# Optimization experiments

Hardware: AMD Instinct MI355X
Metric: run time of the kernel (lower is better)

## Reference

```python
import jax, jax.numpy as jnp
import numpy as np

B, N, F_IN = 8, 1024, 256
N_HEADS, N_HIDDEN = 8, 32  # out_features=256, is_concat=True -> n_hidden = 256//8
NEG_SLOPE = 0.2


def setup_inputs() -> dict:
    key = jax.random.key(0)
    k1, k2, k3 = jax.random.split(key, 3)
    vertex = jax.random.normal(k1, (B, N, F_IN), dtype=jnp.float32)
    # linear_vert.weight.T  (applied as x @ w_vert)
    w_vert = jax.random.normal(k2, (F_IN, N_HEADS * N_HIDDEN), dtype=jnp.float32) / np.sqrt(F_IN)
    # attn linear: [2*n_hidden] -> 1, no bias; shared across heads
    attn_w = jax.random.normal(k3, (2 * N_HIDDEN,), dtype=jnp.float32) / np.sqrt(2 * N_HIDDEN)
    return {"vertex": vertex, "w_vert": w_vert, "attn_w": attn_w}


def reference(vertex, w_vert, attn_w):
    b, n, _ = vertex.shape
    # g_vertex: [b, n, h, d]
    g = jnp.einsum("bni,io->bno", vertex, w_vert).reshape(b, n, N_HEADS, N_HIDDEN)
    # attn(cat([g_i, g_j])) == g_i . w_src + g_j . w_dst  (cat index i = repeat_interleave half)
    w_src, w_dst = attn_w[:N_HIDDEN], attn_w[N_HIDDEN:]
    s_src = jnp.einsum("bnhd,d->bnh", g, w_src)  # [b, n, h]
    s_dst = jnp.einsum("bnhd,d->bnh", g, w_dst)  # [b, n, h]
    # e[b,i,j,h] = LeakyReLU(s_src[b,i,h] + s_dst[b,j,h])
    e = s_src[:, :, None, :] + s_dst[:, None, :, :]
    e = jnp.where(e >= 0, e, NEG_SLOPE * e)
    # softmax over j (dim=-2 after squeeze in the torch code)
    a = jax.nn.softmax(e, axis=2)  # [b, i, j, h]
    # dropout in eval mode = identity
    out = jnp.einsum("bijh,bjhd->bihd", a, g)  # [b, n, h, d]
    return out.reshape(b, n, N_HEADS * N_HIDDEN)
```

## Files before the change

kernel.cpp:

```cpp
#include <hip/hip_runtime.h>
#include <hip/hip_bf16.h>
#include <math.h>

#define F_IN  256
#define NOUT  256
#define NB    8
#define NN    1024
#define NH    8
#define ND    32
#define NROWS (NB * NN)
#define LOG2E 1.44269504f

typedef __attribute__((ext_vector_type(8))) short bf16x8;
typedef __attribute__((ext_vector_type(4))) float f32x4;

__device__ inline unsigned pk_bf16(float a, float b) {
    union { __hip_bfloat162 h2; unsigned u; } c;
    c.h2 = __float22bfloat162_rn(make_float2(a, b));
    return c.u;
}
__device__ inline unsigned short bf16u(float a) {
    union { __hip_bfloat16 h; unsigned short u; } c;
    c.h = __float2bfloat16(a);
    return c.u;
}
__device__ inline float bf2f(unsigned short u) {
    union { unsigned u; float f; } c;
    c.u = ((unsigned)u) << 16;
    return c.f;
}
__device__ inline void split8(const float4 va, const float4 vb,
                              bf16x8& hi, bf16x8& lo) {
    float f[8] = {va.x, va.y, va.z, va.w, vb.x, vb.y, vb.z, vb.w};
    union { bf16x8 v; unsigned u[4]; } H, L;
    #pragma unroll
    for (int i = 0; i < 4; ++i) {
        unsigned short h0 = bf16u(f[2 * i]);
        unsigned short h1 = bf16u(f[2 * i + 1]);
        H.u[i] = (unsigned)h0 | ((unsigned)h1 << 16);
        L.u[i] = pk_bf16(f[2 * i] - bf2f(h0), f[2 * i + 1] - bf2f(h1));
    }
    hi = H.v; lo = L.v;
}

__global__ __launch_bounds__(256) void w_prep_kernel(
    const float* __restrict__ w_vert,
    unsigned short* __restrict__ wT_hi, unsigned short* __restrict__ wT_lo)
{
    __shared__ float wf[64][68];
    const int t  = threadIdx.x;
    const int kt = (blockIdx.x >> 2) * 64;
    const int nt = (blockIdx.x & 3) * 64;
    #pragma unroll
    for (int q = 0; q < 4; ++q) {
        const int kr = (t >> 4) + 16 * q;
        const int nc = (t & 15) * 4;
        float4 v = *(const float4*)&w_vert[(size_t)(kt + kr) * NOUT + nt + nc];
        wf[kr][nc + 0] = v.x; wf[kr][nc + 1] = v.y;
        wf[kr][nc + 2] = v.z; wf[kr][nc + 3] = v.w;
    }
    __syncthreads();
    const int n = t >> 2, ks = (t & 3) * 16;
    unsigned Hs[8], Ls[8];
    #pragma unroll
    for (int i = 0; i < 8; ++i) {
        float x0 = wf[ks + 2 * i][n], x1 = wf[ks + 2 * i + 1][n];
        unsigned short h0 = bf16u(x0), h1 = bf16u(x1);
        Hs[i] = (unsigned)h0 | ((unsigned)h1 << 16);
        Ls[i] = pk_bf16(x0 - bf2f(h0), x1 - bf2f(h1));
    }
    unsigned* ph = (unsigned*)(wT_hi + (size_t)(nt + n) * F_IN + kt + ks);
    unsigned* pl = (unsigned*)(wT_lo + (size_t)(nt + n) * F_IN + kt + ks);
    #pragma unroll
    for (int i = 0; i < 8; ++i) { ph[i] = Hs[i]; pl[i] = Ls[i]; }
}

__global__ __launch_bounds__(256) void gat_gemm_kernel(
    const float* __restrict__ vertex,
    const unsigned short* __restrict__ wT_hi,
    const unsigned short* __restrict__ wT_lo,
    const float* __restrict__ attn_w, unsigned short* __restrict__ gT,
    float* __restrict__ ssT, float* __restrict__ sdT)
{
    __shared__ f32x4 comb[2][4][64];
    const int t = threadIdx.x, lane = t & 63, wv = t >> 6;
    const int mt = wv & 1, kh = wv >> 1;
    const int il = lane & 15, ql = lane >> 4;
    const int h = blockIdx.x, gr0 = blockIdx.y * 64;
    const int b = gr0 >> 10, bh = b * NH + h;

    const float* arow0 = vertex + (size_t)(gr0 + mt * 32 + il) * F_IN + kh * 128 + ql * 8;
    const float* arow1 = arow0 + 16 * F_IN;
    const unsigned short* b0h = wT_hi + (size_t)(h * 32 + il) * F_IN + kh * 128 + ql * 8;
    const unsigned short* b1h = b0h + 16 * F_IN;
    const unsigned short* b0l = wT_lo + (size_t)(h * 32 + il) * F_IN + kh * 128 + ql * 8;
    const unsigned short* b1l = b0l + 16 * F_IN;

    f32x4 c00 = {0.f, 0.f, 0.f, 0.f}, c01 = c00, c10 = c00, c11 = c00;

    #pragma unroll 2
    for (int kk = 0; kk < 128; kk += 32) {
        float4 a0a = *(const float4*)(arow0 + kk);
        float4 a0b = *(const float4*)(arow0 + kk + 4);
        float4 a1a = *(const float4*)(arow1 + kk);
        float4 a1b = *(const float4*)(arow1 + kk + 4);
        bf16x8 bh0 = *(const bf16x8*)(b0h + kk);
        bf16x8 bh1 = *(const bf16x8*)(b1h + kk);
        bf16x8 bl0 = *(const bf16x8*)(b0l + kk);
        bf16x8 bl1 = *(const bf16x8*)(b1l + kk);

        bf16x8 a0hi, a0lo, a1hi, a1lo;
        split8(a0a, a0b, a0hi, a0lo);
        split8(a1a, a1b, a1hi, a1lo);

        c00 = __builtin_amdgcn_mfma_f32_16x16x32_bf16(a0hi, bh0, c00, 0, 0, 0);
        c01 = __builtin_amdgcn_mfma_f32_16x16x32_bf16(a0hi, bh1, c01, 0, 0, 0);
        c10 = __builtin_amdgcn_mfma_f32_16x16x32_bf16(a1hi, bh0, c10, 0, 0, 0);
        c11 = __builtin_amdgcn_mfma_f32_16x16x32_bf16(a1hi, bh1, c11, 0, 0, 0);
        c00 = __builtin_amdgcn_mfma_f32_16x16x32_bf16(a0lo, bh0, c00, 0, 0, 0);
        c01 = __builtin_amdgcn_mfma_f32_16x16x32_bf16(a0lo, bh1, c01, 0, 0, 0);
        c10 = __builtin_amdgcn_mfma_f32_16x16x32_bf16(a1lo, bh0, c10, 0, 0, 0);
        c11 = __builtin_amdgcn_mfma_f32_16x16x32_bf16(a1lo, bh1, c11, 0, 0, 0);
        c00 = __builtin_amdgcn_mfma_f32_16x16x32_bf16(a0hi, bl0, c00, 0, 0, 0);
        c01 = __builtin_amdgcn_mfma_f32_16x16x32_bf16(a0hi, bl1, c01, 0, 0, 0);
        c10 = __builtin_amdgcn_mfma_f32_16x16x32_bf16(a1hi, bl0, c10, 0, 0, 0);
        c11 = __builtin_amdgcn_mfma_f32_16x16x32_bf16(a1hi, bl1, c11, 0, 0, 0);
    }

    if (kh == 1) {
        comb[mt][0][lane] = c00; comb[mt][1][lane] = c01;
        comb[mt][2][lane] = c10; comb[mt][3][lane] = c11;
    }
    __syncthreads();
    if (kh == 0) {
        c00 = c00 + comb[mt][0][lane]; c01 = c01 + comb[mt][1][lane];
        c10 = c10 + comb[mt][2][lane]; c11 = c11 + comb[mt][3][lane];

        const int j0 = (gr0 & 1023) + mt * 32;
        const float wsv0 = attn_w[il],      wsv1 = attn_w[16 + il];
        const float wdv0 = attn_w[ND + il], wdv1 = attn_w[ND + 16 + il];

        #pragma unroll
        for (int g = 0; g < 2; ++g) {
            f32x4 cA = g ? c10 : c00;
            f32x4 cB = g ? c11 : c01;
            const int jr = j0 + g * 16 + ql * 4;

            unsigned g2[2];
            g2[0] = pk_bf16(cA[0], cA[1]); g2[1] = pk_bf16(cA[2], cA[3]);
            *(uint2*)(gT + ((size_t)(bh * ND) + il) * NN + jr) = *(uint2*)g2;
            g2[0] = pk_bf16(cB[0], cB[1]); g2[1] = pk_bf16(cB[2], cB[3]);
            *(uint2*)(gT + ((size_t)(bh * ND) + 16 + il) * NN + jr) = *(uint2*)g2;

            #pragma unroll
            for (int reg = 0; reg < 4; ++reg) {
                float ps = cA[reg] * wsv0 + cB[reg] * wsv1;
                float pd = cA[reg] * wdv0 + cB[reg] * wdv1;
                #pragma unroll
                for (int off = 1; off < 16; off <<= 1) {
                    ps += __shfl_xor(ps, off);
                    pd += __shfl_xor(pd, off);
                }
                if (il == 0) {
                    ssT[bh * NN + jr + reg] = ps;
                    sdT[bh * NN + jr + reg] = pd;
                }
            }
        }
    }
}

__global__ __launch_bounds__(256, 4) void gat_attn_kernel(
    const unsigned short* __restrict__ gT, const float* __restrict__ ssT,
    const float* __restrict__ sdT, float* __restrict__ out)
{
    __shared__ __align__(16) float Bp[NN];
    __shared__ __align__(16) float Bn[NN];
    __shared__ f32x4 ccomb[2][12][64];
    __shared__ float red[4];

    const int bid = blockIdx.x;
    const int bh = bid & 63;
    const int b = bh >> 3, h = bh & 7;
    const int i0 = (bid >> 6) * 64;
    const int t = threadIdx.x, lane = t & 63, jq = t >> 6;
    const int il = lane & 15, ql = lane >> 4;

    float sdv[4]; float M = -3.0e38f;
    #pragma unroll
    for (int q = 0; q < 4; ++q) {
        sdv[q] = sdT[bh * NN + t + 256 * q];
        M = fmaxf(M, sdv[q]);
    }
    #pragma unroll
    for (int off = 32; off >= 1; off >>= 1)
        M = fmaxf(M, __shfl_xor(M, off));
    if (lane == 0) red[jq] = M;
    #pragma unroll
    for (int q = 0; q < 4; ++q) {
        Bp[t + 256 * q] = exp2f(sdv[q] * LOG2E);
        Bn[t + 256 * q] = exp2f(0.2f * LOG2E * sdv[q]);
    }
    __syncthreads();
    M = fmaxf(fmaxf(red[0], red[1]), fmaxf(red[2], red[3]));

    float Ap[4], An[4];
    #pragma unroll
    for (int mt = 0; mt < 4; ++mt) {
        const float si = ssT[bh * NN + i0 + mt * 16 + il];
        float x = si + M; x = fmaxf(x, 0.2f * x);
        const float mk = x * LOG2E;
        Ap[mt] = exp2f(fmaf(si, LOG2E, -mk));
        An[mt] = exp2f(fmaf(0.2f * si, LOG2E, -mk));
    }

    const unsigned short* gb0 = gT + ((size_t)(bh * ND) + il) * NN + jq * 256 + ql * 8;
    const unsigned short* gb1 = gb0 + 16 * NN;
    const float* bpq = Bp + jq * 256 + ql * 8;
    const float* bnq = Bn + jq * 256 + ql * 8;

    union { bf16x8 v; unsigned u[4]; } ones;
    ones.u[0] = ones.u[1] = ones.u[2] = ones.u[3] = 0x3F803F80u;

    f32x4 c0[4], c1[4], cs[4];
    #pragma unroll
    for (int mt = 0; mt < 4; ++mt) {
        c0[mt] = (f32x4){0.f, 0.f, 0.f, 0.f};
        c1[mt] = c0[mt]; cs[mt] = c0[mt];
    }

    #pragma unroll 2
    for (int kk = 0; kk < 256; kk += 32) {
        const float4 p0 = *(const float4*)(bpq + kk);
        const float4 p1 = *(const float4*)(bpq + kk + 4);
        const float4 n0 = *(const float4*)(bnq + kk);
        const float4 n1 = *(const float4*)(bnq + kk + 4);
        const bf16x8 bf0 = *(const bf16x8*)(gb0 + kk);
        const bf16x8 bf1 = *(const bf16x8*)(gb1 + kk);

        float pv[8] = {p0.x, p0.y, p0.z, p0.w, p1.x, p1.y, p1.z, p1.w};
        float nv[8] = {n0.x, n0.y, n0.z, n0.w, n1.x, n1.y, n1.z, n1.w};

        #pragma unroll
        for (int mt = 0; mt < 4; ++mt) {
            float e[8];
            #pragma unroll
            for (int u = 0; u < 8; ++u)
                e[u] = fmaxf(Ap[mt] * pv[u], An[mt] * nv[u]);
            union { bf16x8 v; unsigned u[4]; } af;
            #pragma unroll
            for (int u = 0; u < 4; ++u)
                af.u[u] = pk_bf16(e[2 * u], e[2 * u + 1]);
            c0[mt] = __builtin_amdgcn_mfma_f32_16x16x32_bf16(af.v, bf0, c0[mt], 0, 0, 0);
            c1[mt] = __builtin_amdgcn_mfma_f32_16x16x32_bf16(af.v, bf1, c1[mt], 0, 0, 0);
            cs[mt] = __builtin_amdgcn_mfma_f32_16x16x32_bf16(af.v, ones.v, cs[mt], 0, 0, 0);
        }
    }

    if (jq >= 2) {
        #pragma unroll
        for (int mt = 0; mt < 4; ++mt) {
            ccomb[jq - 2][mt * 3 + 0][lane] = c0[mt];
            ccomb[jq - 2][mt * 3 + 1][lane] = c1[mt];
            ccomb[jq - 2][mt * 3 + 2][lane] = cs[mt];
        }
    }
    __syncthreads();
    if (jq < 2) {
        #pragma unroll
        for (int mt = 0; mt < 4; ++mt) {
            c0[mt] = c0[mt] + ccomb[jq][mt * 3 + 0][lane];
            c1[mt] = c1[mt] + ccomb[jq][mt * 3 + 1][lane];
            cs[mt] = cs[mt] + ccomb[jq][mt * 3 + 2][lane];
        }
    }
    __syncthreads();
    if (jq == 1) {
        #pragma unroll
        for (int mt = 0; mt < 4; ++mt) {
            ccomb[0][mt * 3 + 0][lane] = c0[mt];
            ccomb[0][mt * 3 + 1][lane] = c1[mt];
            ccomb[0][mt * 3 + 2][lane] = cs[mt];
        }
    }
    __syncthreads();
    if (jq == 0) {
        #pragma unroll
        for (int mt = 0; mt < 4; ++mt) {
            c0[mt] = c0[mt] + ccomb[0][mt * 3 + 0][lane];
            c1[mt] = c1[mt] + ccomb[0][mt * 3 + 1][lane];
            cs[mt] = cs[mt] + ccomb[0][mt * 3 + 2][lane];

            float* ob = out + (size_t)(b * NN + i0 + mt * 16 + ql * 4) * NOUT + h * ND + il;
            #pragma unroll
            for (int reg = 0; reg < 4; ++reg) {
                const float r = 1.0f / cs[mt][reg];
                ob[reg * NOUT]      = c0[mt][reg] * r;
                ob[reg * NOUT + 16] = c1[mt][reg] * r;
            }
        }
    }
}

extern "C" void kernel_launch(void* const* d_in, const int* in_sizes, int n_in,
                              void* d_out, int out_size, void* d_ws, size_t ws_size,
                              hipStream_t stream) {
    (void)in_sizes; (void)n_in; (void)out_size; (void)ws_size;
    const float* vertex = (const float*)d_in[0];
    const float* w_vert = (const float*)d_in[1];
    const float* attn_w = (const float*)d_in[2];
    float* out = (float*)d_out;

    char* ws = (char*)d_ws;
    unsigned short* wT_hi = (unsigned short*)ws;
    unsigned short* wT_lo = (unsigned short*)(ws + (128 << 10));
    unsigned short* gT    = (unsigned short*)(ws + (256 << 10));
    float* ssT = (float*)(ws + (256 << 10) + ((size_t)NB * NH * ND * NN * 2));
    float* sdT = ssT + (size_t)NB * NH * NN;

    w_prep_kernel<<<16, 256, 0, stream>>>(w_vert, wT_hi, wT_lo);
    gat_gemm_kernel<<<dim3(NH, 128), 256, 0, stream>>>(vertex, wT_hi, wT_lo,
                                                       attn_w, gT, ssT, sdT);
    gat_attn_kernel<<<1024, 256, 0, stream>>>(gT, ssT, sdT, out);
}
```

Before: 96.72 us.

## Fuse weight bf16 split into GEMM kernel via shared-memory staging

```diff
diff --git a/kernel.cpp b/kernel.cpp
--- a/kernel.cpp
+++ b/kernel.cpp
@@ -43,71 +43,66 @@
     hi = H.v; lo = L.v;
 }
 
-__global__ __launch_bounds__(256) void w_prep_kernel(
-    const float* __restrict__ w_vert,
-    unsigned short* __restrict__ wT_hi, unsigned short* __restrict__ wT_lo)
-{
-    __shared__ float wf[64][68];
-    const int t  = threadIdx.x;
-    const int kt = (blockIdx.x >> 2) * 64;
-    const int nt = (blockIdx.x & 3) * 64;
-    #pragma unroll
-    for (int q = 0; q < 4; ++q) {
-        const int kr = (t >> 4) + 16 * q;
-        const int nc = (t & 15) * 4;
-        float4 v = *(const float4*)&w_vert[(size_t)(kt + kr) * NOUT + nt + nc];
-        wf[kr][nc + 0] = v.x; wf[kr][nc + 1] = v.y;
-        wf[kr][nc + 2] = v.z; wf[kr][nc + 3] = v.w;
-    }
-    __syncthreads();
-    const int n = t >> 2, ks = (t & 3) * 16;
-    unsigned Hs[8], Ls[8];
-    #pragma unroll
-    for (int i = 0; i < 8; ++i) {
-        float x0 = wf[ks + 2 * i][n], x1 = wf[ks + 2 * i + 1][n];
-        unsigned short h0 = bf16u(x0), h1 = bf16u(x1);
-        Hs[i] = (unsigned)h0 | ((unsigned)h1 << 16);
-        Ls[i] = pk_bf16(x0 - bf2f(h0), x1 - bf2f(h1));
-    }
-    unsigned* ph = (unsigned*)(wT_hi + (size_t)(nt + n) * F_IN + kt + ks);
-    unsigned* pl = (unsigned*)(wT_lo + (size_t)(nt + n) * F_IN + kt + ks);
-    #pragma unroll
-    for (int i = 0; i < 8; ++i) { ph[i] = Hs[i]; pl[i] = Ls[i]; }
-}
-
 __global__ __launch_bounds__(256) void gat_gemm_kernel(
-    const float* __restrict__ vertex,
-    const unsigned short* __restrict__ wT_hi,
-    const unsigned short* __restrict__ wT_lo,
+    const float* __restrict__ vertex, const float* __restrict__ w_vert,
     const float* __restrict__ attn_w, unsigned short* __restrict__ gT,
     float* __restrict__ ssT, float* __restrict__ sdT)
 {
-    __shared__ f32x4 comb[2][4][64];
+    __shared__ __align__(16) unsigned short bHi[8192];
+    __shared__ __align__(16) unsigned short bLo[8192];
+    f32x4 (*comb)[4][64] = reinterpret_cast<f32x4(*)[4][64]>(bHi);
+
     const int t = threadIdx.x, lane = t & 63, wv = t >> 6;
     const int mt = wv & 1, kh = wv >> 1;
     const int il = lane & 15, ql = lane >> 4;
     const int h = blockIdx.x, gr0 = blockIdx.y * 64;
     const int b = gr0 >> 10, bh = b * NH + h;
 
+    {
+        const int n  = t & 31;
+        const int kb = t >> 5;
+        const int il_s = n & 15, nt_s = n >> 4;
+        #pragma unroll
+        for (int q = 0; q < 4; ++q) {
+            const int k0 = kb * 8 + 64 * q;
+            const float* wp = w_vert + (size_t)k0 * NOUT + h * 32 + n;
+            float f[8];
+            #pragma unroll
+            for (int j = 0; j < 8; ++j) f[j] = wp[j * NOUT];
+            unsigned hu[4], lu[4];
+            #pragma unroll
+            for (int j2 = 0; j2 < 4; ++j2) {
+                unsigned short h0 = bf16u(f[2 * j2]);
+                unsigned short h1 = bf16u(f[2 * j2 + 1]);
+                hu[j2] = (unsigned)h0 | ((unsigned)h1 << 16);
+                lu[j2] = pk_bf16(f[2 * j2] - bf2f(h0), f[2 * j2 + 1] - bf2f(h1));
+            }
+            const int ktile = k0 >> 5;
+            const int qlb   = (k0 & 31) >> 3;
+            const int off   = (ktile * 2 + nt_s) * 512 + (qlb * 16 + il_s) * 8;
+            *(uint4*)&bHi[off] = *(const uint4*)hu;
+            *(uint4*)&bLo[off] = *(const uint4*)lu;
+        }
+    }
+    __syncthreads();
+
     const float* arow0 = vertex + (size_t)(gr0 + mt * 32 + il) * F_IN + kh * 128 + ql * 8;
     const float* arow1 = arow0 + 16 * F_IN;
-    const unsigned short* b0h = wT_hi + (size_t)(h * 32 + il) * F_IN + kh * 128 + ql * 8;
-    const unsigned short* b1h = b0h + 16 * F_IN;
-    const unsigned short* b0l = wT_lo + (size_t)(h * 32 + il) * F_IN + kh * 128 + ql * 8;
-    const unsigned short* b1l = b0l + 16 * F_IN;
 
     f32x4 c00 = {0.f, 0.f, 0.f, 0.f}, c01 = c00, c10 = c00, c11 = c00;
 
-    #pragma unroll 2
-    for (int kk = 0; kk < 128; kk += 32) {
-        float4 a0a = *(const float4*)(arow0 + kk);
-        float4 a0b = *(const float4*)(arow0 + kk + 4);
-        float4 a1a = *(const float4*)(arow1 + kk);
-        float4 a1b = *(const float4*)(arow1 + kk + 4);
-        bf16x8 bh0 = *(const bf16x8*)(b0h + kk);
-        bf16x8 bh1 = *(const bf16x8*)(b1h + kk);
-        bf16x8 bl0 = *(const bf16x8*)(b0l + kk);
-        bf16x8 bl1 = *(const bf16x8*)(b1l + kk);
+    #pragma unroll
+    for (int kk = 0; kk < 4; ++kk) {
+        float4 a0a = *(const float4*)(arow0 + kk * 32);
+        float4 a0b = *(const float4*)(arow0 + kk * 32 + 4);
+        float4 a1a = *(const float4*)(arow1 + kk * 32);
+        float4 a1b = *(const float4*)(arow1 + kk * 32 + 4);
+
+        const int bkb = (kh * 4 + kk) * 2;
+        bf16x8 bh0 = *(const bf16x8*)&bHi[bkb * 512 + lane * 8];
+        bf16x8 bh1 = *(const bf16x8*)&bHi[(bkb + 1) * 512 + lane * 8];
+        bf16x8 bl0 = *(const bf16x8*)&bLo[bkb * 512 + lane * 8];
+        bf16x8 bl1 = *(const bf16x8*)&bLo[(bkb + 1) * 512 + lane * 8];
 
         bf16x8 a0hi, a0lo, a1hi, a1lo;
         split8(a0a, a0b, a0hi, a0lo);
@@ -127,6 +122,7 @@
         c11 = __builtin_amdgcn_mfma_f32_16x16x32_bf16(a1hi, bl1, c11, 0, 0, 0);
     }
 
+    __syncthreads();
     if (kh == 1) {
         comb[mt][0][lane] = c00; comb[mt][1][lane] = c01;
         comb[mt][2][lane] = c10; comb[mt][3][lane] = c11;
@@ -312,14 +308,11 @@
     float* out = (float*)d_out;
 
     char* ws = (char*)d_ws;
-    unsigned short* wT_hi = (unsigned short*)ws;
-    unsigned short* wT_lo = (unsigned short*)(ws + (128 << 10));
-    unsigned short* gT    = (unsigned short*)(ws + (256 << 10));
-    float* ssT = (float*)(ws + (256 << 10) + ((size_t)NB * NH * ND * NN * 2));
+    unsigned short* gT = (unsigned short*)ws;
+    float* ssT = (float*)(ws + ((size_t)NB * NH * ND * NN * 2));
     float* sdT = ssT + (size_t)NB * NH * NN;
 
-    w_prep_kernel<<<16, 256, 0, stream>>>(w_vert, wT_hi, wT_lo);
-    gat_gemm_kernel<<<dim3(NH, 128), 256, 0, stream>>>(vertex, wT_hi, wT_lo,
-                                                       attn_w, gT, ssT, sdT);
+    gat_gemm_kernel<<<dim3(NH, 128), 256, 0, stream>>>(vertex, w_vert, attn_w,
+                                                       gT, ssT, sdT);
     gat_attn_kernel<<<1024, 256, 0, stream>>>(gT, ssT, sdT, out);
 }
```

After: 89.78 us. 1.08x faster.
